# Optimization experiments

Measured on AMD Instinct MI355X. Metric: run time of the kernel, lower is better.

The kernel has to match this reference:

```python
import jax, jax.numpy as jnp
import numpy as np

B, H, N, D, A = 96, 100, 128, 768, 256  # batch, max_history_num, news_num, news_embedding_dim, attention_dim


def setup_inputs() -> dict:
    key = jax.random.key(0)
    ks = jax.random.split(key, 6)
    w = lambda k, shape: jax.random.normal(k, shape, jnp.float32) * 0.02
    return {
        "history_embedding": jax.random.normal(ks[0], (B, H, D), jnp.float32),
        "candidate_news_representation": jax.random.normal(ks[1], (B, N, D), jnp.float32),
        "W_l": w(ks[2], (D, D)),              # SAGEConv lin_l (neighbor) weight
        "b_l": jnp.zeros((D,), jnp.float32),  # SAGEConv lin_l bias
        "W_r": w(ks[3], (D, D)),              # SAGEConv lin_r (root) weight, bias=False
        "W_K": w(ks[4], (A, D)),              # K Linear, bias=False
        "W_Q": w(ks[5], (A, D)),              # Q Linear, bias=True
        "b_Q": jnp.zeros((A,), jnp.float32),
    }


def reference(history_embedding, candidate_news_representation, W_l, b_l, W_r, W_K, W_Q, b_Q):
    b, h, d = history_embedding.shape
    n = candidate_news_representation.shape[1]
    a_dim = W_K.shape[0]

    # --- GraphSAGE (1 layer SAGEConv, mean aggr, PyG node_dim=-2) ---
    # edge_index: src = user rows 0..b-1 (indexing the history dim!), dst = 0..h-1.
    # Every dst h receives all srcs 0..b-1, so the mean-aggregated neighbor feature is
    # mean over the first b history slots, identical for every h.
    neigh = jnp.mean(history_embedding[:, :b, :], axis=1)  # [b, d]
    gcn = (
        jnp.einsum("bhd,ed->bhe", history_embedding, W_r)
        + (neigh @ W_l.T + b_l)[:, None, :]
    )  # [b, h, d]

    # --- K/Q attention pooling over history ---
    user_rep = gcn[:, 0, :]                                  # [b, d] (gcn_feature[:, :1, :])
    K = jnp.einsum("bhd,ad->bha", gcn, W_K)                  # [b, h, A]
    Q = user_rep @ W_Q.T + b_Q                               # [b, A]
    scores = jnp.einsum("bha,ba->bh", K, Q) / jnp.sqrt(jnp.float32(a_dim))
    alpha = jax.nn.softmax(scores, axis=1)                   # [b, h]
    out = jnp.einsum("bh,bhd->bd", alpha, gcn)               # [b, d]

    # In torch, news_rep/user_rep2 are expand()ed over news_num with identical content,
    # so the per-candidate outputs are all equal: broadcast instead of recomputing.
    return jnp.broadcast_to(out[:, None, :], (b, n, d))
```

## Files before the change

kernel.cpp:

```cpp
#include <hip/hip_runtime.h>
#include <hip/hip_bf16.h>

#define BB 96
#define HH 100
#define NN 128
#define DD 768
#define AA 256

static __device__ __forceinline__ float dot4(float4 a, float4 b) {
  return a.x * b.x + a.y * b.y + a.z * b.z + a.w * b.w;
}

__global__ void t_trans(const float* __restrict__ src, float* __restrict__ dst,
                        int R, int C) {
  __shared__ float tile[32][33];
  int tx = threadIdx.x & 31, ty = threadIdx.x >> 5;
  int c0 = blockIdx.x * 32, r0 = blockIdx.y * 32;
#pragma unroll
  for (int k = 0; k < 4; ++k)
    tile[ty + 8 * k][tx] = src[(size_t)(r0 + ty + 8 * k) * C + c0 + tx];
  __syncthreads();
#pragma unroll
  for (int k = 0; k < 4; ++k)
    dst[(size_t)(c0 + ty + 8 * k) * R + r0 + tx] = tile[tx][ty + 8 * k];
}

__global__ void k_neigh(const float* __restrict__ hist, float* __restrict__ neighp) {
  int b = blockIdx.x, hg = blockIdx.y;
  int t = threadIdx.x;
  const float* hb = hist + (size_t)b * HH * DD + (size_t)hg * 12 * DD + t * 4;
  float4 acc = make_float4(0.f, 0.f, 0.f, 0.f);
#pragma unroll
  for (int i = 0; i < 12; ++i) {
    float4 x = *(const float4*)(hb + (size_t)i * DD);
    acc.x += x.x; acc.y += x.y; acc.z += x.z; acc.w += x.w;
  }
  *(float4*)(neighp + ((size_t)hg * BB + b) * DD + t * 4) = acc;
}

__global__ void k_nl_u0(const float* __restrict__ neighp, const float* __restrict__ hist,
                        const float* __restrict__ Wl, const float* __restrict__ bl,
                        const float* __restrict__ Wr,
                        float* __restrict__ nl, float* __restrict__ u0) {
  int e0 = blockIdx.x * 32;
  int b0 = blockIdx.y * 3;
  int lane = threadIdx.x & 63, wave = threadIdx.x >> 6;
  float4 xn[3][3], xh[3][3];
#pragma unroll
  for (int bi = 0; bi < 3; ++bi) {
    int b = b0 + bi;
#pragma unroll
    for (int jj = 0; jj < 3; ++jj) {
      int idx = lane + 64 * jj;
      float4 s = make_float4(0.f, 0.f, 0.f, 0.f);
#pragma unroll
      for (int g = 0; g < 8; ++g) {
        float4 x = ((const float4*)(neighp + ((size_t)g * BB + b) * DD))[idx];
        s.x += x.x; s.y += x.y; s.z += x.z; s.w += x.w;
      }
      xn[bi][jj] = make_float4(s.x * (1.f / 96.f), s.y * (1.f / 96.f),
                               s.z * (1.f / 96.f), s.w * (1.f / 96.f));
      xh[bi][jj] = ((const float4*)(hist + (size_t)b * HH * DD))[idx];
    }
  }
  for (int i = 0; i < 8; ++i) {
    int e = e0 + wave * 8 + i;
    const float4* wl4 = (const float4*)(Wl + (size_t)e * DD);
    const float4* wr4 = (const float4*)(Wr + (size_t)e * DD);
    float pl[3] = {0.f, 0.f, 0.f}, pr[3] = {0.f, 0.f, 0.f};
#pragma unroll
    for (int jj = 0; jj < 3; ++jj) {
      float4 wl = wl4[lane + 64 * jj];
      float4 wr = wr4[lane + 64 * jj];
#pragma unroll
      for (int bi = 0; bi < 3; ++bi) {
        pl[bi] += dot4(wl, xn[bi][jj]);
        pr[bi] += dot4(wr, xh[bi][jj]);
      }
    }
#pragma unroll
    for (int bi = 0; bi < 3; ++bi) {
      float pp = pl[bi], qq = pr[bi];
      for (int off = 32; off; off >>= 1) {
        pp += __shfl_down(pp, off, 64);
        qq += __shfl_down(qq, off, 64);
      }
      if (lane == 0) {
        float nle = pp + bl[e];
        nl[(size_t)(b0 + bi) * DD + e] = nle;
        u0[(size_t)(b0 + bi) * DD + e] = qq + nle;
      }
    }
  }
}

__global__ void k_q(const float* __restrict__ u0, const float* __restrict__ WQ,
                    const float* __restrict__ bQ, float* __restrict__ Qm) {
  int a0 = blockIdx.x * 32;
  int b0 = blockIdx.y * 3;
  int lane = threadIdx.x & 63, wave = threadIdx.x >> 6;
  float4 x[3][3];
#pragma unroll
  for (int bi = 0; bi < 3; ++bi)
#pragma unroll
    for (int jj = 0; jj < 3; ++jj)
      x[bi][jj] = ((const float4*)(u0 + (size_t)(b0 + bi) * DD))[lane + 64 * jj];
  for (int i = 0; i < 8; ++i) {
    int a = a0 + wave * 8 + i;
    const float4* w4 = (const float4*)(WQ + (size_t)a * DD);
    float p[3] = {0.f, 0.f, 0.f};
#pragma unroll
    for (int jj = 0; jj < 3; ++jj) {
      float4 w = w4[lane + 64 * jj];
#pragma unroll
      for (int bi = 0; bi < 3; ++bi) p[bi] += dot4(w, x[bi][jj]);
    }
#pragma unroll
    for (int bi = 0; bi < 3; ++bi) {
      float pp = p[bi];
      for (int off = 32; off; off >>= 1) pp += __shfl_down(pp, off, 64);
      if (lane == 0) Qm[(size_t)(b0 + bi) * AA + a] = pp + bQ[a];
    }
  }
}

__global__ void k_qk(const float* __restrict__ Qm, const float* __restrict__ WKT,
                     float* __restrict__ qk) {
  int d0 = blockIdx.x * 32;
  int b0 = blockIdx.y * 3;
  int lane = threadIdx.x & 63, wave = threadIdx.x >> 6;
  float4 x[3];
#pragma unroll
  for (int bi = 0; bi < 3; ++bi)
    x[bi] = ((const float4*)(Qm + (size_t)(b0 + bi) * AA))[lane];
  for (int i = 0; i < 8; ++i) {
    int d = d0 + wave * 8 + i;
    float4 w = ((const float4*)(WKT + (size_t)d * AA))[lane];
    float p[3];
#pragma unroll
    for (int bi = 0; bi < 3; ++bi) p[bi] = dot4(w, x[bi]);
#pragma unroll
    for (int bi = 0; bi < 3; ++bi) {
      float pp = p[bi];
      for (int off = 32; off; off >>= 1) pp += __shfl_down(pp, off, 64);
      if (lane == 0) qk[(size_t)(b0 + bi) * DD + d] = pp;
    }
  }
}

__global__ void k_v(const float* __restrict__ qk, const float* __restrict__ WrT,
                    float* __restrict__ vv) {
  int d0 = blockIdx.x * 32;
  int b0 = blockIdx.y * 3;
  int lane = threadIdx.x & 63, wave = threadIdx.x >> 6;
  float4 x[3][3];
#pragma unroll
  for (int bi = 0; bi < 3; ++bi)
#pragma unroll
    for (int jj = 0; jj < 3; ++jj)
      x[bi][jj] = ((const float4*)(qk + (size_t)(b0 + bi) * DD))[lane + 64 * jj];
  for (int i = 0; i < 8; ++i) {
    int d = d0 + wave * 8 + i;
    const float4* w4 = (const float4*)(WrT + (size_t)d * DD);
    float p[3] = {0.f, 0.f, 0.f};
#pragma unroll
    for (int jj = 0; jj < 3; ++jj) {
      float4 w = w4[lane + 64 * jj];
#pragma unroll
      for (int bi = 0; bi < 3; ++bi) p[bi] += dot4(w, x[bi][jj]);
    }
#pragma unroll
    for (int bi = 0; bi < 3; ++bi) {
      float pp = p[bi];
      for (int off = 32; off; off >>= 1) pp += __shfl_down(pp, off, 64);
      if (lane == 0) vv[(size_t)(b0 + bi) * DD + d] = pp * (1.f / 16.f);
    }
  }
}

__global__ void k_scores(const float* __restrict__ hist, const float* __restrict__ vv,
                         float* __restrict__ sc) {
  int b = blockIdx.x, hg = blockIdx.y;
  int lane = threadIdx.x & 63, wave = threadIdx.x >> 6;
  float4 v[3];
  const float4* vb = (const float4*)(vv + (size_t)b * DD);
#pragma unroll
  for (int jj = 0; jj < 3; ++jj) v[jj] = vb[lane + 64 * jj];
  const float* hb = hist + (size_t)b * HH * DD;
  for (int i = 0; i < 5; ++i) {
    int h = hg * 20 + wave * 5 + i;
    const float4* r = (const float4*)(hb + (size_t)h * DD);
    float p = 0.f;
#pragma unroll
    for (int jj = 0; jj < 3; ++jj) p += dot4(r[lane + 64 * jj], v[jj]);
    for (int off = 32; off; off >>= 1) p += __shfl_down(p, off, 64);
    if (lane == 0) sc[b * 128 + h] = p;
  }
}

__global__ void k_wsum(const float* __restrict__ hist, const float* __restrict__ sc,
                       float* __restrict__ wsum) {
  int b = blockIdx.x;
  int e = blockIdx.y * 256 + threadIdx.x;
  __shared__ float sal[HH];
  __shared__ float s_inv;
  if (threadIdx.x < HH) sal[threadIdx.x] = sc[b * 128 + threadIdx.x];
  __syncthreads();
  if (threadIdx.x == 0) {
    float m = -1e30f;
    for (int h = 0; h < HH; ++h) m = fmaxf(m, sal[h]);
    float s = 0.f;
    for (int h = 0; h < HH; ++h) { float ex = __expf(sal[h] - m); sal[h] = ex; s += ex; }
    s_inv = 1.f / s;
  }
  __syncthreads();
  float inv = s_inv;
  float acc = 0.f;
  const float* hb = hist + (size_t)b * HH * DD + e;
  for (int h = 0; h < HH; h += 4) {
    float v0 = hb[(size_t)(h + 0) * DD];
    float v1 = hb[(size_t)(h + 1) * DD];
    float v2 = hb[(size_t)(h + 2) * DD];
    float v3 = hb[(size_t)(h + 3) * DD];
    acc += sal[h + 0] * v0 + sal[h + 1] * v1 + sal[h + 2] * v2 + sal[h + 3] * v3;
  }
  wsum[(size_t)b * DD + e] = acc * inv;
}

__global__ void k_orow(const float* __restrict__ wsum, const float* __restrict__ Wr,
                       const float* __restrict__ nl, float* __restrict__ orow) {
  int d0 = blockIdx.x * 32;
  int b0 = blockIdx.y * 3;
  int lane = threadIdx.x & 63, wave = threadIdx.x >> 6;
  float4 x[3][3];
#pragma unroll
  for (int bi = 0; bi < 3; ++bi)
#pragma unroll
    for (int jj = 0; jj < 3; ++jj)
      x[bi][jj] = ((const float4*)(wsum + (size_t)(b0 + bi) * DD))[lane + 64 * jj];
  for (int i = 0; i < 8; ++i) {
    int d = d0 + wave * 8 + i;
    const float4* w4 = (const float4*)(Wr + (size_t)d * DD);
    float p[3] = {0.f, 0.f, 0.f};
#pragma unroll
    for (int jj = 0; jj < 3; ++jj) {
      float4 w = w4[lane + 64 * jj];
#pragma unroll
      for (int bi = 0; bi < 3; ++bi) p[bi] += dot4(w, x[bi][jj]);
    }
#pragma unroll
    for (int bi = 0; bi < 3; ++bi) {
      float pp = p[bi];
      for (int off = 32; off; off >>= 1) pp += __shfl_down(pp, off, 64);
      if (lane == 0)
        orow[(size_t)(b0 + bi) * DD + d] = pp + nl[(size_t)(b0 + bi) * DD + d];
    }
  }
}

__global__ void k_write(const float* __restrict__ orow, float* __restrict__ out) {
  size_t t = (size_t)blockIdx.x * 256 + threadIdx.x;
  int d4 = (int)(t % (DD / 4));
  int bn = (int)(t / (DD / 4));
  int b = bn >> 7;
  float4 v = *(const float4*)(orow + (size_t)b * DD + d4 * 4);
  *(float4*)(out + (size_t)bn * DD + d4 * 4) = v;
}

extern "C" void kernel_launch(void* const* d_in, const int* in_sizes, int n_in,
                              void* d_out, int out_size, void* d_ws, size_t ws_size,
                              hipStream_t stream) {
  const float *hist = nullptr, *Wl = nullptr, *Wr = nullptr, *WK = nullptr,
              *WQ = nullptr, *bl = nullptr, *bQ = nullptr;
  int seenDxD = 0, seenAxD = 0;
  for (int i = 0; i < n_in; ++i) {
    int s = in_sizes[i];
    const float* p = (const float*)d_in[i];
    if (s == BB * HH * DD) hist = p;
    else if (s == BB * NN * DD) {  }
    else if (s == DD * DD) { if (seenDxD++ == 0) Wl = p; else Wr = p; }
    else if (s == AA * DD) { if (seenAxD++ == 0) WK = p; else WQ = p; }
    else if (s == DD) bl = p;
    else if (s == AA) bQ = p;
  }

  float* ws = (float*)d_ws;
  float* neighp = ws + 0;
  float* WrT    = ws + 589824;
  float* WKT    = ws + 1179648;
  float* nl     = ws + 1376256;
  float* u0     = ws + 1449984;
  float* Qm     = ws + 1523712;
  float* qk     = ws + 1548288;
  float* vv     = ws + 1622016;
  float* sc     = ws + 1695744;
  float* wsum   = ws + 1708032;
  float* orow   = ws + 1781760;
  float* out = (float*)d_out;

  t_trans <<<dim3(24, 24), dim3(256), 0, stream>>>(Wr, WrT, DD, DD);
  t_trans <<<dim3(24, 8),  dim3(256), 0, stream>>>(WK, WKT, AA, DD);
  k_neigh <<<dim3(BB, 8),  dim3(192), 0, stream>>>(hist, neighp);
  k_nl_u0 <<<dim3(24, 32), dim3(256), 0, stream>>>(neighp, hist, Wl, bl, Wr, nl, u0);
  k_q     <<<dim3(8, 32),  dim3(256), 0, stream>>>(u0, WQ, bQ, Qm);
  k_qk    <<<dim3(24, 32), dim3(256), 0, stream>>>(Qm, WKT, qk);
  k_v     <<<dim3(24, 32), dim3(256), 0, stream>>>(qk, WrT, vv);
  k_scores<<<dim3(BB, 5),  dim3(256), 0, stream>>>(hist, vv, sc);
  k_wsum  <<<dim3(BB, 3),  dim3(256), 0, stream>>>(hist, sc, wsum);
  k_orow  <<<dim3(24, 32), dim3(256), 0, stream>>>(wsum, Wr, nl, orow);
  k_write <<<dim3(9216),   dim3(256), 0, stream>>>(orow, out);
}
```

Baseline: 109.2 us.

## Fuse prep, query-chain and attention kernels into per-batch fused kernels

Merges the two weight transposes and the neighbour-sum kernel into one launch. The Q, QK and V projection chain is fused into a single kernel with one 1024-thread block per batch that keeps intermediates in shared memory. Scores, softmax and the weighted sum are fused into another per-batch kernel that uses a wave-level softmax. This cuts the launch count from eleven to six, but each block now streams the full WQ/WKT/WrT weights instead of sharing them across three batches, and only 96 blocks run on the fused stages.

```diff
diff --git a/kernel.cpp b/kernel.cpp
--- a/kernel.cpp
+++ b/kernel.cpp
@@ -11,31 +11,39 @@
   return a.x * b.x + a.y * b.y + a.z * b.z + a.w * b.w;
 }
 
-__global__ void t_trans(const float* __restrict__ src, float* __restrict__ dst,
-                        int R, int C) {
+__global__ void k_prep(const float* __restrict__ Wr, const float* __restrict__ WK,
+                       const float* __restrict__ hist,
+                       float* __restrict__ WrT, float* __restrict__ WKT,
+                       float* __restrict__ neighp) {
   __shared__ float tile[32][33];
-  int tx = threadIdx.x & 31, ty = threadIdx.x >> 5;
-  int c0 = blockIdx.x * 32, r0 = blockIdx.y * 32;
-#pragma unroll
-  for (int k = 0; k < 4; ++k)
-    tile[ty + 8 * k][tx] = src[(size_t)(r0 + ty + 8 * k) * C + c0 + tx];
-  __syncthreads();
-#pragma unroll
-  for (int k = 0; k < 4; ++k)
-    dst[(size_t)(c0 + ty + 8 * k) * R + r0 + tx] = tile[tx][ty + 8 * k];
-}
-
-__global__ void k_neigh(const float* __restrict__ hist, float* __restrict__ neighp) {
-  int b = blockIdx.x, hg = blockIdx.y;
-  int t = threadIdx.x;
-  const float* hb = hist + (size_t)b * HH * DD + (size_t)hg * 12 * DD + t * 4;
-  float4 acc = make_float4(0.f, 0.f, 0.f, 0.f);
-#pragma unroll
-  for (int i = 0; i < 12; ++i) {
-    float4 x = *(const float4*)(hb + (size_t)i * DD);
-    acc.x += x.x; acc.y += x.y; acc.z += x.z; acc.w += x.w;
-  }
-  *(float4*)(neighp + ((size_t)hg * BB + b) * DD + t * 4) = acc;
+  int bid = blockIdx.x;
+  if (bid < 768) {
+    const float* src; float* dst; int R, C, bx, by;
+    if (bid < 576) { src = Wr; dst = WrT; R = DD; C = DD; bx = bid % 24; by = bid / 24; }
+    else { int id = bid - 576; src = WK; dst = WKT; R = AA; C = DD; bx = id % 24; by = id / 24; }
+    int tx = threadIdx.x & 31, ty = threadIdx.x >> 5;
+    int c0 = bx * 32, r0 = by * 32;
+#pragma unroll
+    for (int k = 0; k < 4; ++k)
+      tile[ty + 8 * k][tx] = src[(size_t)(r0 + ty + 8 * k) * C + c0 + tx];
+    __syncthreads();
+#pragma unroll
+    for (int k = 0; k < 4; ++k)
+      dst[(size_t)(c0 + ty + 8 * k) * R + r0 + tx] = tile[tx][ty + 8 * k];
+  } else {
+    int id = bid - 768;
+    int b = id % BB, hg = id / BB;
+    int t = threadIdx.x;
+    if (t >= 192) return;
+    const float* hb = hist + (size_t)b * HH * DD + (size_t)hg * 12 * DD + t * 4;
+    float4 acc = make_float4(0.f, 0.f, 0.f, 0.f);
+#pragma unroll
+    for (int i = 0; i < 12; ++i) {
+      float4 x = *(const float4*)(hb + (size_t)i * DD);
+      acc.x += x.x; acc.y += x.y; acc.z += x.z; acc.w += x.w;
+    }
+    *(float4*)(neighp + ((size_t)hg * BB + b) * DD + t * 4) = acc;
+  }
 }
 
 __global__ void k_nl_u0(const float* __restrict__ neighp, const float* __restrict__ hist,
@@ -94,137 +102,105 @@
   }
 }
 
-__global__ void k_q(const float* __restrict__ u0, const float* __restrict__ WQ,
-                    const float* __restrict__ bQ, float* __restrict__ Qm) {
-  int a0 = blockIdx.x * 32;
-  int b0 = blockIdx.y * 3;
-  int lane = threadIdx.x & 63, wave = threadIdx.x >> 6;
-  float4 x[3][3];
-#pragma unroll
-  for (int bi = 0; bi < 3; ++bi)
-#pragma unroll
-    for (int jj = 0; jj < 3; ++jj)
-      x[bi][jj] = ((const float4*)(u0 + (size_t)(b0 + bi) * DD))[lane + 64 * jj];
-  for (int i = 0; i < 8; ++i) {
-    int a = a0 + wave * 8 + i;
-    const float4* w4 = (const float4*)(WQ + (size_t)a * DD);
-    float p[3] = {0.f, 0.f, 0.f};
-#pragma unroll
-    for (int jj = 0; jj < 3; ++jj) {
-      float4 w = w4[lane + 64 * jj];
-#pragma unroll
-      for (int bi = 0; bi < 3; ++bi) p[bi] += dot4(w, x[bi][jj]);
-    }
-#pragma unroll
-    for (int bi = 0; bi < 3; ++bi) {
-      float pp = p[bi];
-      for (int off = 32; off; off >>= 1) pp += __shfl_down(pp, off, 64);
-      if (lane == 0) Qm[(size_t)(b0 + bi) * AA + a] = pp + bQ[a];
-    }
-  }
-}
-
-__global__ void k_qk(const float* __restrict__ Qm, const float* __restrict__ WKT,
-                     float* __restrict__ qk) {
-  int d0 = blockIdx.x * 32;
-  int b0 = blockIdx.y * 3;
-  int lane = threadIdx.x & 63, wave = threadIdx.x >> 6;
-  float4 x[3];
-#pragma unroll
-  for (int bi = 0; bi < 3; ++bi)
-    x[bi] = ((const float4*)(Qm + (size_t)(b0 + bi) * AA))[lane];
-  for (int i = 0; i < 8; ++i) {
-    int d = d0 + wave * 8 + i;
-    float4 w = ((const float4*)(WKT + (size_t)d * AA))[lane];
-    float p[3];
-#pragma unroll
-    for (int bi = 0; bi < 3; ++bi) p[bi] = dot4(w, x[bi]);
-#pragma unroll
-    for (int bi = 0; bi < 3; ++bi) {
-      float pp = p[bi];
-      for (int off = 32; off; off >>= 1) pp += __shfl_down(pp, off, 64);
-      if (lane == 0) qk[(size_t)(b0 + bi) * DD + d] = pp;
-    }
-  }
-}
-
-__global__ void k_v(const float* __restrict__ qk, const float* __restrict__ WrT,
-                    float* __restrict__ vv) {
-  int d0 = blockIdx.x * 32;
-  int b0 = blockIdx.y * 3;
-  int lane = threadIdx.x & 63, wave = threadIdx.x >> 6;
-  float4 x[3][3];
-#pragma unroll
-  for (int bi = 0; bi < 3; ++bi)
-#pragma unroll
-    for (int jj = 0; jj < 3; ++jj)
-      x[bi][jj] = ((const float4*)(qk + (size_t)(b0 + bi) * DD))[lane + 64 * jj];
-  for (int i = 0; i < 8; ++i) {
-    int d = d0 + wave * 8 + i;
-    const float4* w4 = (const float4*)(WrT + (size_t)d * DD);
-    float p[3] = {0.f, 0.f, 0.f};
-#pragma unroll
-    for (int jj = 0; jj < 3; ++jj) {
-      float4 w = w4[lane + 64 * jj];
-#pragma unroll
-      for (int bi = 0; bi < 3; ++bi) p[bi] += dot4(w, x[bi][jj]);
-    }
-#pragma unroll
-    for (int bi = 0; bi < 3; ++bi) {
-      float pp = p[bi];
-      for (int off = 32; off; off >>= 1) pp += __shfl_down(pp, off, 64);
-      if (lane == 0) vv[(size_t)(b0 + bi) * DD + d] = pp * (1.f / 16.f);
-    }
-  }
-}
-
-__global__ void k_scores(const float* __restrict__ hist, const float* __restrict__ vv,
-                         float* __restrict__ sc) {
-  int b = blockIdx.x, hg = blockIdx.y;
-  int lane = threadIdx.x & 63, wave = threadIdx.x >> 6;
-  float4 v[3];
-  const float4* vb = (const float4*)(vv + (size_t)b * DD);
-#pragma unroll
-  for (int jj = 0; jj < 3; ++jj) v[jj] = vb[lane + 64 * jj];
-  const float* hb = hist + (size_t)b * HH * DD;
-  for (int i = 0; i < 5; ++i) {
-    int h = hg * 20 + wave * 5 + i;
-    const float4* r = (const float4*)(hb + (size_t)h * DD);
-    float p = 0.f;
-#pragma unroll
-    for (int jj = 0; jj < 3; ++jj) p += dot4(r[lane + 64 * jj], v[jj]);
-    for (int off = 32; off; off >>= 1) p += __shfl_down(p, off, 64);
-    if (lane == 0) sc[b * 128 + h] = p;
-  }
-}
-
-__global__ void k_wsum(const float* __restrict__ hist, const float* __restrict__ sc,
-                       float* __restrict__ wsum) {
+__global__ void __launch_bounds__(1024)
+k_head(const float* __restrict__ u0, const float* __restrict__ WQ,
+       const float* __restrict__ bQ, const float* __restrict__ WKT,
+       const float* __restrict__ WrT, float* __restrict__ vv) {
   int b = blockIdx.x;
-  int e = blockIdx.y * 256 + threadIdx.x;
-  __shared__ float sal[HH];
-  __shared__ float s_inv;
-  if (threadIdx.x < HH) sal[threadIdx.x] = sc[b * 128 + threadIdx.x];
-  __syncthreads();
-  if (threadIdx.x == 0) {
-    float m = -1e30f;
-    for (int h = 0; h < HH; ++h) m = fmaxf(m, sal[h]);
-    float s = 0.f;
-    for (int h = 0; h < HH; ++h) { float ex = __expf(sal[h] - m); sal[h] = ex; s += ex; }
-    s_inv = 1.f / s;
-  }
-  __syncthreads();
-  float inv = s_inv;
-  float acc = 0.f;
-  const float* hb = hist + (size_t)b * HH * DD + e;
-  for (int h = 0; h < HH; h += 4) {
-    float v0 = hb[(size_t)(h + 0) * DD];
-    float v1 = hb[(size_t)(h + 1) * DD];
-    float v2 = hb[(size_t)(h + 2) * DD];
-    float v3 = hb[(size_t)(h + 3) * DD];
-    acc += sal[h + 0] * v0 + sal[h + 1] * v1 + sal[h + 2] * v2 + sal[h + 3] * v3;
-  }
-  wsum[(size_t)b * DD + e] = acc * inv;
+  int tid = threadIdx.x, lane = tid & 63, wave = tid >> 6;
+  __shared__ __align__(16) float s_u0[DD];
+  __shared__ __align__(16) float s_Q[AA];
+  __shared__ __align__(16) float s_qk[DD];
+  if (tid < 192)
+    ((float4*)s_u0)[tid] = ((const float4*)(u0 + (size_t)b * DD))[tid];
+  __syncthreads();
+  {
+    float4 x0 = ((const float4*)s_u0)[lane];
+    float4 x1 = ((const float4*)s_u0)[lane + 64];
+    float4 x2 = ((const float4*)s_u0)[lane + 128];
+    for (int i = 0; i < 16; ++i) {
+      int a = wave * 16 + i;
+      const float4* w4 = (const float4*)(WQ + (size_t)a * DD);
+      float p = dot4(w4[lane], x0) + dot4(w4[lane + 64], x1) + dot4(w4[lane + 128], x2);
+      for (int off = 32; off; off >>= 1) p += __shfl_down(p, off, 64);
+      if (lane == 0) s_Q[a] = p + bQ[a];
+    }
+  }
+  __syncthreads();
+  {
+    float4 x = ((const float4*)s_Q)[lane];
+    for (int i = 0; i < 48; ++i) {
+      int d = wave * 48 + i;
+      float4 w = ((const float4*)(WKT + (size_t)d * AA))[lane];
+      float p = dot4(w, x);
+      for (int off = 32; off; off >>= 1) p += __shfl_down(p, off, 64);
+      if (lane == 0) s_qk[d] = p;
+    }
+  }
+  __syncthreads();
+  {
+    float4 x0 = ((const float4*)s_qk)[lane];
+    float4 x1 = ((const float4*)s_qk)[lane + 64];
+    float4 x2 = ((const float4*)s_qk)[lane + 128];
+    for (int i = 0; i < 48; ++i) {
+      int c = wave * 48 + i;
+      const float4* w4 = (const float4*)(WrT + (size_t)c * DD);
+      float p = dot4(w4[lane], x0) + dot4(w4[lane + 64], x1) + dot4(w4[lane + 128], x2);
+      for (int off = 32; off; off >>= 1) p += __shfl_down(p, off, 64);
+      if (lane == 0) vv[(size_t)b * DD + c] = p * (1.f / 16.f);
+    }
+  }
+}
+
+__global__ void __launch_bounds__(1024)
+k_attn(const float* __restrict__ hist, const float* __restrict__ vv,
+       float* __restrict__ wsum) {
+  int b = blockIdx.x;
+  int tid = threadIdx.x, lane = tid & 63, wave = tid >> 6;
+  __shared__ __align__(16) float s_v[DD];
+  __shared__ float s_al[HH];
+  if (tid < 192)
+    ((float4*)s_v)[tid] = ((const float4*)(vv + (size_t)b * DD))[tid];
+  __syncthreads();
+  {
+    float4 v0 = ((const float4*)s_v)[lane];
+    float4 v1 = ((const float4*)s_v)[lane + 64];
+    float4 v2 = ((const float4*)s_v)[lane + 128];
+    const float* hb = hist + (size_t)b * HH * DD;
+    for (int h = wave; h < HH; h += 16) {
+      const float4* r = (const float4*)(hb + (size_t)h * DD);
+      float p = dot4(r[lane], v0) + dot4(r[lane + 64], v1) + dot4(r[lane + 128], v2);
+      for (int off = 32; off; off >>= 1) p += __shfl_down(p, off, 64);
+      if (lane == 0) s_al[h] = p;
+    }
+  }
+  __syncthreads();
+  if (wave == 0) {
+    float x0 = (lane < HH) ? s_al[lane] : -1e30f;
+    float x1 = (lane + 64 < HH) ? s_al[lane + 64] : -1e30f;
+    float m = fmaxf(x0, x1);
+    for (int off = 32; off; off >>= 1) m = fmaxf(m, __shfl_xor(m, off, 64));
+    float e0 = (lane < HH) ? __expf(x0 - m) : 0.f;
+    float e1 = (lane + 64 < HH) ? __expf(x1 - m) : 0.f;
+    float s = e0 + e1;
+    for (int off = 32; off; off >>= 1) s += __shfl_xor(s, off, 64);
+    float inv = 1.f / s;
+    if (lane < HH) s_al[lane] = e0 * inv;
+    if (lane + 64 < HH) s_al[lane + 64] = e1 * inv;
+  }
+  __syncthreads();
+  if (tid < DD) {
+    const float* hb = hist + (size_t)b * HH * DD + tid;
+    float acc = 0.f;
+    for (int h = 0; h < HH; h += 4) {
+      float v0 = hb[(size_t)(h + 0) * DD];
+      float v1 = hb[(size_t)(h + 1) * DD];
+      float v2 = hb[(size_t)(h + 2) * DD];
+      float v3 = hb[(size_t)(h + 3) * DD];
+      acc += s_al[h + 0] * v0 + s_al[h + 1] * v1 + s_al[h + 2] * v2 + s_al[h + 3] * v3;
+    }
+    wsum[(size_t)b * DD + tid] = acc;
+  }
 }
 
 __global__ void k_orow(const float* __restrict__ wsum, const float* __restrict__ Wr,
@@ -290,23 +266,15 @@
   float* WKT    = ws + 1179648;
   float* nl     = ws + 1376256;
   float* u0     = ws + 1449984;
-  float* Qm     = ws + 1523712;
-  float* qk     = ws + 1548288;
-  float* vv     = ws + 1622016;
-  float* sc     = ws + 1695744;
-  float* wsum   = ws + 1708032;
-  float* orow   = ws + 1781760;
+  float* vv     = ws + 1523712;
+  float* wsum   = ws + 1597440;
+  float* orow   = ws + 1671168;
   float* out = (float*)d_out;
 
-  t_trans <<<dim3(24, 24), dim3(256), 0, stream>>>(Wr, WrT, DD, DD);
-  t_trans <<<dim3(24, 8),  dim3(256), 0, stream>>>(WK, WKT, AA, DD);
-  k_neigh <<<dim3(BB, 8),  dim3(192), 0, stream>>>(hist, neighp);
-  k_nl_u0 <<<dim3(24, 32), dim3(256), 0, stream>>>(neighp, hist, Wl, bl, Wr, nl, u0);
-  k_q     <<<dim3(8, 32),  dim3(256), 0, stream>>>(u0, WQ, bQ, Qm);
-  k_qk    <<<dim3(24, 32), dim3(256), 0, stream>>>(Qm, WKT, qk);
-  k_v     <<<dim3(24, 32), dim3(256), 0, stream>>>(qk, WrT, vv);
-  k_scores<<<dim3(BB, 5),  dim3(256), 0, stream>>>(hist, vv, sc);
-  k_wsum  <<<dim3(BB, 3),  dim3(256), 0, stream>>>(hist, sc, wsum);
-  k_orow  <<<dim3(24, 32), dim3(256), 0, stream>>>(wsum, Wr, nl, orow);
-  k_write <<<dim3(9216),   dim3(256), 0, stream>>>(orow, out);
-}
+  k_prep  <<<dim3(1536),   dim3(256),  0, stream>>>(Wr, WK, hist, WrT, WKT, neighp);
+  k_nl_u0 <<<dim3(24, 32), dim3(256),  0, stream>>>(neighp, hist, Wl, bl, Wr, nl, u0);
+  k_head  <<<dim3(BB),     dim3(1024), 0, stream>>>(u0, WQ, bQ, WKT, WrT, vv);
+  k_attn  <<<dim3(BB),     dim3(1024), 0, stream>>>(hist, vv, wsum);
+  k_orow  <<<dim3(24, 32), dim3(256),  0, stream>>>(wsum, Wr, nl, orow);
+  k_write <<<dim3(9216),   dim3(256),  0, stream>>>(orow, out);
+}
```

Result: slower. 126.4 us (+15.7%).

## Fuse transposes with neighbor mean and fold broadcast write into output GEMV

Applied to the files above, without the earlier changes.

Merges the two weight transposes and the history-mean reduction into one prep kernel, and computes the full mean per batch in a single block instead of eight partial blocks. The final output-row GEMV now stages its results in shared memory and writes the broadcast over candidates directly, which removes the separate write kernel and the intermediate orow buffer. The aim is fewer launches and less intermediate global traffic. The trade-off is less parallelism in the mean (96 blocks each reading 96 rows), and the output GEMV blocks now also carry the large broadcast store.

```diff
diff --git a/kernel.cpp b/kernel.cpp
--- a/kernel.cpp
+++ b/kernel.cpp
@@ -11,34 +11,46 @@
   return a.x * b.x + a.y * b.y + a.z * b.z + a.w * b.w;
 }
 
-__global__ void t_trans(const float* __restrict__ src, float* __restrict__ dst,
-                        int R, int C) {
+__global__ void k_prep(const float* __restrict__ Wr, const float* __restrict__ WK,
+                       const float* __restrict__ hist,
+                       float* __restrict__ WrT, float* __restrict__ WKT,
+                       float* __restrict__ neigh) {
   __shared__ float tile[32][33];
-  int tx = threadIdx.x & 31, ty = threadIdx.x >> 5;
-  int c0 = blockIdx.x * 32, r0 = blockIdx.y * 32;
-#pragma unroll
-  for (int k = 0; k < 4; ++k)
-    tile[ty + 8 * k][tx] = src[(size_t)(r0 + ty + 8 * k) * C + c0 + tx];
-  __syncthreads();
-#pragma unroll
-  for (int k = 0; k < 4; ++k)
-    dst[(size_t)(c0 + ty + 8 * k) * R + r0 + tx] = tile[tx][ty + 8 * k];
-}
-
-__global__ void k_neigh(const float* __restrict__ hist, float* __restrict__ neighp) {
-  int b = blockIdx.x, hg = blockIdx.y;
-  int t = threadIdx.x;
-  const float* hb = hist + (size_t)b * HH * DD + (size_t)hg * 12 * DD + t * 4;
-  float4 acc = make_float4(0.f, 0.f, 0.f, 0.f);
-#pragma unroll
-  for (int i = 0; i < 12; ++i) {
-    float4 x = *(const float4*)(hb + (size_t)i * DD);
-    acc.x += x.x; acc.y += x.y; acc.z += x.z; acc.w += x.w;
-  }
-  *(float4*)(neighp + ((size_t)hg * BB + b) * DD + t * 4) = acc;
-}
-
-__global__ void k_nl_u0(const float* __restrict__ neighp, const float* __restrict__ hist,
+  int bid = blockIdx.x;
+  if (bid < 768) {
+    const float* src; float* dst; int R, C, bx, by;
+    if (bid < 576) { src = Wr; dst = WrT; R = DD; C = DD; bx = bid % 24; by = bid / 24; }
+    else { int id = bid - 576; src = WK; dst = WKT; R = AA; C = DD; bx = id % 24; by = id / 24; }
+    int tx = threadIdx.x & 31, ty = threadIdx.x >> 5;
+    int c0 = bx * 32, r0 = by * 32;
+#pragma unroll
+    for (int k = 0; k < 4; ++k)
+      tile[ty + 8 * k][tx] = src[(size_t)(r0 + ty + 8 * k) * C + c0 + tx];
+    __syncthreads();
+#pragma unroll
+    for (int k = 0; k < 4; ++k)
+      dst[(size_t)(c0 + ty + 8 * k) * R + r0 + tx] = tile[tx][ty + 8 * k];
+  } else {
+    int b = bid - 768;
+    int t = threadIdx.x;
+    if (t >= 192) return;
+    const float* hb = hist + (size_t)b * HH * DD + t * 4;
+    float4 a0 = make_float4(0.f, 0.f, 0.f, 0.f);
+    float4 a1 = make_float4(0.f, 0.f, 0.f, 0.f);
+#pragma unroll 8
+    for (int h = 0; h < 96; h += 2) {
+      float4 x = *(const float4*)(hb + (size_t)h * DD);
+      float4 y = *(const float4*)(hb + (size_t)(h + 1) * DD);
+      a0.x += x.x; a0.y += x.y; a0.z += x.z; a0.w += x.w;
+      a1.x += y.x; a1.y += y.y; a1.z += y.z; a1.w += y.w;
+    }
+    float4 m = make_float4((a0.x + a1.x) * (1.f / 96.f), (a0.y + a1.y) * (1.f / 96.f),
+                           (a0.z + a1.z) * (1.f / 96.f), (a0.w + a1.w) * (1.f / 96.f));
+    *(float4*)(neigh + (size_t)b * DD + t * 4) = m;
+  }
+}
+
+__global__ void k_nl_u0(const float* __restrict__ neigh, const float* __restrict__ hist,
                         const float* __restrict__ Wl, const float* __restrict__ bl,
                         const float* __restrict__ Wr,
                         float* __restrict__ nl, float* __restrict__ u0) {
@@ -52,14 +64,7 @@
 #pragma unroll
     for (int jj = 0; jj < 3; ++jj) {
       int idx = lane + 64 * jj;
-      float4 s = make_float4(0.f, 0.f, 0.f, 0.f);
-#pragma unroll
-      for (int g = 0; g < 8; ++g) {
-        float4 x = ((const float4*)(neighp + ((size_t)g * BB + b) * DD))[idx];
-        s.x += x.x; s.y += x.y; s.z += x.z; s.w += x.w;
-      }
-      xn[bi][jj] = make_float4(s.x * (1.f / 96.f), s.y * (1.f / 96.f),
-                               s.z * (1.f / 96.f), s.w * (1.f / 96.f));
+      xn[bi][jj] = ((const float4*)(neigh + (size_t)b * DD))[idx];
       xh[bi][jj] = ((const float4*)(hist + (size_t)b * HH * DD))[idx];
     }
   }
@@ -227,11 +232,12 @@
   wsum[(size_t)b * DD + e] = acc * inv;
 }
 
-__global__ void k_orow(const float* __restrict__ wsum, const float* __restrict__ Wr,
-                       const float* __restrict__ nl, float* __restrict__ orow) {
+__global__ void k_orow_write(const float* __restrict__ wsum, const float* __restrict__ Wr,
+                             const float* __restrict__ nl, float* __restrict__ out) {
   int d0 = blockIdx.x * 32;
   int b0 = blockIdx.y * 3;
   int lane = threadIdx.x & 63, wave = threadIdx.x >> 6;
+  __shared__ __align__(16) float s_o[3][32];
   float4 x[3][3];
 #pragma unroll
   for (int bi = 0; bi < 3; ++bi)
@@ -253,18 +259,20 @@
       float pp = p[bi];
       for (int off = 32; off; off >>= 1) pp += __shfl_down(pp, off, 64);
       if (lane == 0)
-        orow[(size_t)(b0 + bi) * DD + d] = pp + nl[(size_t)(b0 + bi) * DD + d];
-    }
-  }
-}
-
-__global__ void k_write(const float* __restrict__ orow, float* __restrict__ out) {
-  size_t t = (size_t)blockIdx.x * 256 + threadIdx.x;
-  int d4 = (int)(t % (DD / 4));
-  int bn = (int)(t / (DD / 4));
-  int b = bn >> 7;
-  float4 v = *(const float4*)(orow + (size_t)b * DD + d4 * 4);
-  *(float4*)(out + (size_t)bn * DD + d4 * 4) = v;
+        s_o[bi][wave * 8 + i] = pp + nl[(size_t)(b0 + bi) * DD + d];
+    }
+  }
+  __syncthreads();
+  float4* out4 = (float4*)out;
+  int d4 = d0 >> 2;
+#pragma unroll
+  for (int k = 0; k < 12; ++k) {
+    int g = threadIdx.x + (k << 8);
+    int seg = g >> 3, off = g & 7;
+    int bi = seg >> 7, n = seg & 127;
+    float4 val = *(const float4*)&s_o[bi][off * 4];
+    out4[((size_t)(b0 + bi) * NN + n) * (DD / 4) + d4 + off] = val;
+  }
 }
 
 extern "C" void kernel_launch(void* const* d_in, const int* in_sizes, int n_in,
@@ -285,28 +293,24 @@
   }
 
   float* ws = (float*)d_ws;
-  float* neighp = ws + 0;
-  float* WrT    = ws + 589824;
-  float* WKT    = ws + 1179648;
-  float* nl     = ws + 1376256;
-  float* u0     = ws + 1449984;
-  float* Qm     = ws + 1523712;
-  float* qk     = ws + 1548288;
-  float* vv     = ws + 1622016;
-  float* sc     = ws + 1695744;
-  float* wsum   = ws + 1708032;
-  float* orow   = ws + 1781760;
+  float* WrT   = ws + 0;
+  float* WKT   = ws + 589824;
+  float* neigh = ws + 786432;
+  float* nl    = ws + 860160;
+  float* u0    = ws + 933888;
+  float* Qm    = ws + 1007616;
+  float* qk    = ws + 1032192;
+  float* vv    = ws + 1105920;
+  float* sc    = ws + 1179648;
+  float* wsum  = ws + 1191936;
   float* out = (float*)d_out;
 
-  t_trans <<<dim3(24, 24), dim3(256), 0, stream>>>(Wr, WrT, DD, DD);
-  t_trans <<<dim3(24, 8),  dim3(256), 0, stream>>>(WK, WKT, AA, DD);
-  k_neigh <<<dim3(BB, 8),  dim3(192), 0, stream>>>(hist, neighp);
-  k_nl_u0 <<<dim3(24, 32), dim3(256), 0, stream>>>(neighp, hist, Wl, bl, Wr, nl, u0);
-  k_q     <<<dim3(8, 32),  dim3(256), 0, stream>>>(u0, WQ, bQ, Qm);
-  k_qk    <<<dim3(24, 32), dim3(256), 0, stream>>>(Qm, WKT, qk);
-  k_v     <<<dim3(24, 32), dim3(256), 0, stream>>>(qk, WrT, vv);
-  k_scores<<<dim3(BB, 5),  dim3(256), 0, stream>>>(hist, vv, sc);
-  k_wsum  <<<dim3(BB, 3),  dim3(256), 0, stream>>>(hist, sc, wsum);
-  k_orow  <<<dim3(24, 32), dim3(256), 0, stream>>>(wsum, Wr, nl, orow);
-  k_write <<<dim3(9216),   dim3(256), 0, stream>>>(orow, out);
-}
+  k_prep      <<<dim3(864),    dim3(256), 0, stream>>>(Wr, WK, hist, WrT, WKT, neigh);
+  k_nl_u0     <<<dim3(24, 32), dim3(256), 0, stream>>>(neigh, hist, Wl, bl, Wr, nl, u0);
+  k_q         <<<dim3(8, 32),  dim3(256), 0, stream>>>(u0, WQ, bQ, Qm);
+  k_qk        <<<dim3(24, 32), dim3(256), 0, stream>>>(Qm, WKT, qk);
+  k_v         <<<dim3(24, 32), dim3(256), 0, stream>>>(qk, WrT, vv);
+  k_scores    <<<dim3(96, 5),  dim3(256), 0, stream>>>(hist, vv, sc);
+  k_wsum      <<<dim3(96, 3),  dim3(256), 0, stream>>>(hist, sc, wsum);
+  k_orow_write<<<dim3(24, 32), dim3(256), 0, stream>>>(wsum, Wr, nl, out);
+}
```

Measured after the change: 95.31 us. 1.15x faster.
